# Performance work log

Measured on AMD Instinct MI355X. Metric: run time of the kernel, lower is better.

## Reference

```python
import jax, jax.numpy as jnp
import numpy as np

B, S, N, D, H, M, P_OFF = 16, 4, 2048, 128, 16, 4096, 4092


def setup_inputs() -> dict:
    key = jax.random.key(0)
    ks = jax.random.split(key, 6)
    return {
        "X": jax.random.normal(ks[0], (B, S, N), dtype=jnp.float32),
        "W_q": jax.random.normal(ks[1], (N, N), dtype=jnp.float32) * 0.02,
        "W_k": jax.random.normal(ks[2], (N, N), dtype=jnp.float32) * 0.02,
        "W_v": jax.random.normal(ks[3], (N, N), dtype=jnp.float32) * 0.02,
        "cache_K": jax.random.normal(ks[4], (B, H, M, D), dtype=jnp.float32),
        "cache_V": jax.random.normal(ks[5], (B, H, M, D), dtype=jnp.float32),
        "P": P_OFF,
    }


def reference(X, W_q, W_k, W_v, cache_K, cache_V, P):
    b, s, n = X.shape
    _, h, m, d = cache_K.shape
    # RMSNorm (no eps, no learned scale, matching the source)
    variance = jnp.mean(X * X, axis=-1, keepdims=True)
    X_norm = X * jax.lax.rsqrt(variance)
    # QKV projections -> [b, h, s, d]
    Q = (X_norm @ W_q).reshape(b, s, h, d).transpose(0, 2, 1, 3)
    K = (X_norm @ W_k).reshape(b, s, h, d).transpose(0, 2, 1, 3)
    V = (X_norm @ W_v).reshape(b, s, h, d).transpose(0, 2, 1, 3)
    # KV-cache write at static offset P
    cK = cache_K.at[:, :, P:P + s, :].set(K)
    cV = cache_V.at[:, :, P:P + s, :].set(V)
    # Attention over full cache (note: source applies no 1/sqrt(d) scale)
    scores = jnp.einsum("bhsd,bhmd->bhsm", Q, cK)
    attn = jax.nn.softmax(scores, axis=-1)
    O = jnp.einsum("bhsm,bhmd->bhsd", attn, cV)
    return O.transpose(0, 2, 1, 3).reshape(b, s, n)
```

## Files before the change

kernel.cpp:

```cpp
#include <hip/hip_runtime.h>
#include <hip/hip_bf16.h>
#include <math.h>

#define NB 16
#define NS 4
#define NN 2048
#define ND 128
#define NH 16
#define NM 4096
#define NCHK 8
#define CHROWS 512

#define XN_OFF   0u
#define Q_OFF    131072u
#define K_OFF    262144u
#define V_OFF    393216u
#define OP_OFF   524288u
#define ML_OFF   1572864u
#define PART_OFF 1589248u

__global__ __launch_bounds__(256) void k_rmsnorm(const float* __restrict__ X,
                                                 float* __restrict__ ws) {
    const int row = blockIdx.x;
    const int tid = threadIdx.x;
    const float* xr = X + (size_t)row * NN;
    float4 a = *(const float4*)(xr + tid * 4);
    float4 b = *(const float4*)(xr + 1024 + tid * 4);
    float ss = a.x*a.x + a.y*a.y + a.z*a.z + a.w*a.w
             + b.x*b.x + b.y*b.y + b.z*b.z + b.w*b.w;
    #pragma unroll
    for (int off = 32; off; off >>= 1) ss += __shfl_xor(ss, off);
    __shared__ float ls[4];
    if ((tid & 63) == 0) ls[tid >> 6] = ss;
    __syncthreads();
    const float r = rsqrtf((ls[0] + ls[1] + ls[2] + ls[3]) * (1.0f / NN));
    float* o = ws + XN_OFF + (size_t)row * NN;
    *(float4*)(o + tid * 4)        = make_float4(a.x*r, a.y*r, a.z*r, a.w*r);
    *(float4*)(o + 1024 + tid * 4) = make_float4(b.x*r, b.y*r, b.z*r, b.w*r);
}

__global__ __launch_bounds__(256) void k_qkv(const float* __restrict__ Wq,
                                             const float* __restrict__ Wk,
                                             const float* __restrict__ Wv,
                                             float* __restrict__ ws) {
    __shared__ float xsT[64][68];
    __shared__ float wt[64][132];
    const int ct    = blockIdx.x;
    const int which = blockIdx.y;
    const int kc    = blockIdx.z;
    const float* __restrict__ W = (which == 0) ? Wq : (which == 1) ? Wk : Wv;
    const int tid = threadIdx.x;
    const int c0  = ct * 128;
    const int rg  = tid >> 5;
    const int cg  = tid & 31;
    const float* xn = ws + XN_OFF;

    float4 acc[8];
    #pragma unroll
    for (int i = 0; i < 8; i++) acc[i] = make_float4(0.f, 0.f, 0.f, 0.f);

    for (int s = 0; s < 4; s++) {
        const int k0 = kc * 256 + s * 64;
        __syncthreads();
        {
            const int r  = tid >> 2;
            const int q4 = tid & 3;
            #pragma unroll
            for (int i = 0; i < 4; i++) {
                const int f4 = q4 + i * 4;
                float4 v = *(const float4*)(xn + (size_t)r * NN + k0 + f4 * 4);
                xsT[f4 * 4 + 0][r] = v.x;
                xsT[f4 * 4 + 1][r] = v.y;
                xsT[f4 * 4 + 2][r] = v.z;
                xsT[f4 * 4 + 3][r] = v.w;
            }
        }
        {
            #pragma unroll
            for (int j8 = 0; j8 < 8; j8++) {
                const int kk  = j8 * 8 + (tid >> 5);
                const int f4c = tid & 31;
                float4 v = *(const float4*)(W + (size_t)(k0 + kk) * NN + c0 + f4c * 4);
                *(float4*)&wt[kk][f4c * 4] = v;
            }
        }
        __syncthreads();
        #pragma unroll 8
        for (int kk = 0; kk < 64; kk++) {
            const float4 x0 = *(const float4*)&xsT[kk][rg * 8];
            const float4 x1 = *(const float4*)&xsT[kk][rg * 8 + 4];
            const float4 w4 = *(const float4*)&wt[kk][cg * 4];
            acc[0].x += x0.x*w4.x; acc[0].y += x0.x*w4.y; acc[0].z += x0.x*w4.z; acc[0].w += x0.x*w4.w;
            acc[1].x += x0.y*w4.x; acc[1].y += x0.y*w4.y; acc[1].z += x0.y*w4.z; acc[1].w += x0.y*w4.w;
            acc[2].x += x0.z*w4.x; acc[2].y += x0.z*w4.y; acc[2].z += x0.z*w4.z; acc[2].w += x0.z*w4.w;
            acc[3].x += x0.w*w4.x; acc[3].y += x0.w*w4.y; acc[3].z += x0.w*w4.z; acc[3].w += x0.w*w4.w;
            acc[4].x += x1.x*w4.x; acc[4].y += x1.x*w4.y; acc[4].z += x1.x*w4.z; acc[4].w += x1.x*w4.w;
            acc[5].x += x1.y*w4.x; acc[5].y += x1.y*w4.y; acc[5].z += x1.y*w4.z; acc[5].w += x1.y*w4.w;
            acc[6].x += x1.z*w4.x; acc[6].y += x1.z*w4.y; acc[6].z += x1.z*w4.z; acc[6].w += x1.z*w4.w;
            acc[7].x += x1.w*w4.x; acc[7].y += x1.w*w4.y; acc[7].z += x1.w*w4.z; acc[7].w += x1.w*w4.w;
        }
    }
    float* po = ws + PART_OFF + (size_t)(kc * 3 + which) * 131072u;
    #pragma unroll
    for (int i = 0; i < 8; i++)
        *(float4*)(po + (size_t)(rg * 8 + i) * NN + c0 + cg * 4) = acc[i];
}

__global__ __launch_bounds__(256) void k_reduce(float* __restrict__ ws) {
    const int idx = blockIdx.x * 256 + threadIdx.x;
    const int which = idx >> 15;
    const int off   = idx & 32767;
    float4 s = make_float4(0.f, 0.f, 0.f, 0.f);
    #pragma unroll
    for (int kcc = 0; kcc < 8; kcc++) {
        const float4 v = *(const float4*)(ws + PART_OFF
                         + (size_t)(kcc * 3 + which) * 131072u + (size_t)off * 4);
        s.x += v.x; s.y += v.y; s.z += v.z; s.w += v.w;
    }
    *(float4*)(ws + Q_OFF + (size_t)which * 131072u + (size_t)off * 4) = s;
}

__global__ __launch_bounds__(256) void k_attn(const float* __restrict__ cK,
                                              const float* __restrict__ cV,
                                              const int* __restrict__ Pp,
                                              float* __restrict__ ws) {
    const int ch = blockIdx.x, h = blockIdx.y, b = blockIdx.z;
    const int tid = threadIdx.x;
    const int wv = tid >> 6, lane = tid & 63;
    const int P = *Pp;
    __shared__ float Ks[2][64 * 128];
    __shared__ float Qs[4][128] __attribute__((aligned(16)));
    __shared__ float ps[64][4] __attribute__((aligned(16)));
    __shared__ float facs[4] __attribute__((aligned(16)));
    __shared__ float Ow[4][4][128];
    __shared__ float mls[4][2];

    if (tid < 128) {
        const int q = tid >> 5, d = (tid & 31) * 4;
        *(float4*)&Qs[q][d] =
            *(const float4*)(ws + Q_OFF + (size_t)(b * 4 + q) * NN + h * 128 + d);
    }

    const float* kbase = cK + (size_t)(b * NH + h) * NM * ND;
    const float* vbase = cV + (size_t)(b * NH + h) * NM * ND;
    const float* knew  = ws + K_OFF;
    const float* vnew  = ws + V_OFF;
    const int mb0 = ch * CHROWS;

    auto STAGE = [&](int tt, int bufi) {
        const int mb = mb0 + tt * 64;
        #pragma unroll
        for (int i = 0; i < 8; i++) {
            const int g0  = (wv * 8 + i) * 64;
            const int g   = g0 + lane;
            const int row = g >> 5;
            const int c4  = g & 31;
            const int csw = c4 ^ (row & 7);
            const int mrow = mb + row;
            const float* src;
            if (mrow >= P && mrow < P + NS)
                src = knew + (size_t)(b * 4 + (mrow - P)) * NN + h * 128 + csw * 4;
            else
                src = kbase + (size_t)mrow * ND + csw * 4;
            __builtin_amdgcn_global_load_lds(
                (const __attribute__((address_space(1))) void*)src,
                (__attribute__((address_space(3))) void*)(&Ks[bufi][g0 * 4]),
                16, 0, 0);
        }
    };

    float m_run = -INFINITY, l_run = 0.f;
    float2 Oa[4];
    #pragma unroll
    for (int q = 0; q < 4; q++) Oa[q] = make_float2(0.f, 0.f);

    STAGE(0, 0);
    __syncthreads();

    for (int t = 0; t < 8; t++) {
        const int cur = t & 1;
        if (t < 7) STAGE(t + 1, cur ^ 1);

        const float* kr = &Ks[cur][lane * 128];
        const int s7 = lane & 7;
        float s = 0.f;
        #pragma unroll
        for (int d4 = 0; d4 < 32; d4++) {
            const float4 k4 = *(const float4*)&kr[(d4 ^ s7) * 4];
            const float4 q4 = *(const float4*)&Qs[wv][d4 * 4];
            s += k4.x*q4.x + k4.y*q4.y + k4.z*q4.z + k4.w*q4.w;
        }
        float wm = s;
        #pragma unroll
        for (int off = 32; off; off >>= 1) wm = fmaxf(wm, __shfl_xor(wm, off));
        const float mn  = fmaxf(m_run, wm);
        const float fac = __expf(m_run - mn);
        m_run = mn;
        const float p = __expf(s - mn);
        l_run = l_run * fac + p;
        ps[lane][wv] = p;
        if (lane == 0) facs[wv] = fac;
        asm volatile("s_waitcnt lgkmcnt(0)" ::: "memory");
        __builtin_amdgcn_s_barrier();
        __builtin_amdgcn_sched_barrier(0);

        const float4 fq = *(const float4*)&facs[0];
        Oa[0].x *= fq.x; Oa[0].y *= fq.x;
        Oa[1].x *= fq.y; Oa[1].y *= fq.y;
        Oa[2].x *= fq.z; Oa[2].y *= fq.z;
        Oa[3].x *= fq.w; Oa[3].y *= fq.w;
        const int r0 = wv * 16;
        #pragma unroll 4
        for (int r = 0; r < 16; r++) {
            const int mr = mb0 + t * 64 + r0 + r;
            const float* vp = (mr >= P && mr < P + NS)
                            ? vnew + (size_t)(b * 4 + (mr - P)) * NN + h * 128
                            : vbase + (size_t)mr * ND;
            const float2 v2 = *(const float2*)(vp + lane * 2);
            const float4 pr = *(const float4*)&ps[r0 + r][0];
            Oa[0].x += pr.x * v2.x; Oa[0].y += pr.x * v2.y;
            Oa[1].x += pr.y * v2.x; Oa[1].y += pr.y * v2.y;
            Oa[2].x += pr.z * v2.x; Oa[2].y += pr.z * v2.y;
            Oa[3].x += pr.w * v2.x; Oa[3].y += pr.w * v2.y;
        }
        __syncthreads();
    }

    #pragma unroll
    for (int off = 32; off; off >>= 1) l_run += __shfl_xor(l_run, off);
    #pragma unroll
    for (int q = 0; q < 4; q++)
        *(float2*)&Ow[wv][q][lane * 2] = Oa[q];
    if (lane == 0) { mls[wv][0] = m_run; mls[wv][1] = l_run; }
    __syncthreads();

    const int q = wv;
    const int d0 = lane * 2;
    float o0 = 0.f, o1 = 0.f;
    #pragma unroll
    for (int w2 = 0; w2 < 4; w2++) {
        o0 += Ow[w2][q][d0];
        o1 += Ow[w2][q][d0 + 1];
    }
    const size_t bh = (size_t)(b * NH + h);
    const size_t pidx = ((bh * NCHK + ch) * 4 + q) * 128 + d0;
    ws[OP_OFF + pidx]     = o0;
    ws[OP_OFF + pidx + 1] = o1;
    if (lane == 0) {
        const size_t mi = ((bh * NCHK + ch) * 4 + q) * 2;
        ws[ML_OFF + mi]     = mls[q][0];
        ws[ML_OFF + mi + 1] = mls[q][1];
    }
}

__global__ __launch_bounds__(256) void k_comb(const float* __restrict__ ws,
                                              float* __restrict__ out) {
    const int bh = blockIdx.x;
    const int b = bh >> 4, h = bh & 15;
    const int tid = threadIdx.x;
    const int q = tid >> 6, d0 = (tid & 63) * 2;
    float ms = -INFINITY;
    #pragma unroll
    for (int c = 0; c < NCHK; c++)
        ms = fmaxf(ms, ws[ML_OFF + (((size_t)bh * NCHK + c) * 4 + q) * 2]);
    float o0 = 0.f, o1 = 0.f, den = 0.f;
    #pragma unroll
    for (int c = 0; c < NCHK; c++) {
        const size_t mi = (((size_t)bh * NCHK + c) * 4 + q) * 2;
        float e = __expf(ws[ML_OFF + mi] - ms);
        den += e * ws[ML_OFF + mi + 1];
        const size_t pi = (((size_t)bh * NCHK + c) * 4 + q) * 128 + d0;
        o0 += e * ws[OP_OFF + pi];
        o1 += e * ws[OP_OFF + pi + 1];
    }
    const float inv = 1.0f / den;
    const size_t oi = (size_t)(b * 4 + q) * NN + h * 128 + d0;
    *(float2*)(out + oi) = make_float2(o0 * inv, o1 * inv);
}

extern "C" void kernel_launch(void* const* d_in, const int* in_sizes, int n_in,
                              void* d_out, int out_size, void* d_ws, size_t ws_size,
                              hipStream_t stream) {
    const float* X  = (const float*)d_in[0];
    const float* Wq = (const float*)d_in[1];
    const float* Wk = (const float*)d_in[2];
    const float* Wv = (const float*)d_in[3];
    const float* cK = (const float*)d_in[4];
    const float* cV = (const float*)d_in[5];
    const int*   Pp = (const int*)d_in[6];
    float* ws = (float*)d_ws;
    float* out = (float*)d_out;

    hipLaunchKernelGGL(k_rmsnorm, dim3(64), dim3(256), 0, stream, X, ws);
    hipLaunchKernelGGL(k_qkv, dim3(16, 3, 8), dim3(256), 0, stream, Wq, Wk, Wv, ws);
    hipLaunchKernelGGL(k_reduce, dim3(384), dim3(256), 0, stream, ws);
    hipLaunchKernelGGL(k_attn, dim3(NCHK, NH, NB), dim3(256), 0, stream, cK, cV, Pp, ws);
    hipLaunchKernelGGL(k_comb, dim3(NB * NH), dim3(256), 0, stream, ws, out);
}
```

Before: 265.7 us.

## Stage V tiles through LDS asynchronously and double split-K in QKV projection

The attention kernel now prefetches V rows into double-buffered LDS alongside K with asynchronous global-to-LDS loads, replacing the synchronous per-row global V reads in the PV loop. Tiles shrink to 32 rows so both K and V buffers fit, and the QK dot product is split across half-waves then combined with a shuffle. Separately, the QKV projection uses 16 K-chunks instead of 8 to expose more blocks, at the cost of twice the partial-sum traffic in the reduce kernel. The partial buffer also doubles in size, which relies on the workspace being large enough.

```diff
diff --git a/kernel.cpp b/kernel.cpp
--- a/kernel.cpp
+++ b/kernel.cpp
@@ -10,6 +10,9 @@
 #define NM 4096
 #define NCHK 8
 #define CHROWS 512
+#define TROWS 32
+#define NT 16
+#define NKC 16
 
 #define XN_OFF   0u
 #define Q_OFF    131072u
@@ -59,8 +62,8 @@
     #pragma unroll
     for (int i = 0; i < 8; i++) acc[i] = make_float4(0.f, 0.f, 0.f, 0.f);
 
-    for (int s = 0; s < 4; s++) {
-        const int k0 = kc * 256 + s * 64;
+    for (int s = 0; s < 2; s++) {
+        const int k0 = kc * 128 + s * 64;
         __syncthreads();
         {
             const int r  = tid >> 2;
@@ -112,7 +115,7 @@
     const int off   = idx & 32767;
     float4 s = make_float4(0.f, 0.f, 0.f, 0.f);
     #pragma unroll
-    for (int kcc = 0; kcc < 8; kcc++) {
+    for (int kcc = 0; kcc < NKC; kcc++) {
         const float4 v = *(const float4*)(ws + PART_OFF
                          + (size_t)(kcc * 3 + which) * 131072u + (size_t)off * 4);
         s.x += v.x; s.y += v.y; s.z += v.z; s.w += v.w;
@@ -127,10 +130,12 @@
     const int ch = blockIdx.x, h = blockIdx.y, b = blockIdx.z;
     const int tid = threadIdx.x;
     const int wv = tid >> 6, lane = tid & 63;
+    const int half = lane >> 5, r32 = lane & 31;
     const int P = *Pp;
-    __shared__ float Ks[2][64 * 128];
+    __shared__ float Ks[2][TROWS * 128];
+    __shared__ float Vs[2][TROWS * 128];
     __shared__ float Qs[4][128] __attribute__((aligned(16)));
-    __shared__ float ps[64][4] __attribute__((aligned(16)));
+    __shared__ float ps[TROWS][4] __attribute__((aligned(16)));
     __shared__ float facs[4] __attribute__((aligned(16)));
     __shared__ float Ow[4][4][128];
     __shared__ float mls[4][2];
@@ -148,25 +153,38 @@
     const int mb0 = ch * CHROWS;
 
     auto STAGE = [&](int tt, int bufi) {
-        const int mb = mb0 + tt * 64;
-        #pragma unroll
-        for (int i = 0; i < 8; i++) {
-            const int g0  = (wv * 8 + i) * 64;
+        const int mb = mb0 + tt * TROWS;
+        #pragma unroll
+        for (int i = 0; i < 4; i++) {
+            const int g0  = (wv * 4 + i) * 64;
             const int g   = g0 + lane;
             const int row = g >> 5;
             const int c4  = g & 31;
             const int csw = c4 ^ (row & 7);
             const int mrow = mb + row;
-            const float* src;
-            if (mrow >= P && mrow < P + NS)
-                src = knew + (size_t)(b * 4 + (mrow - P)) * NN + h * 128 + csw * 4;
-            else
-                src = kbase + (size_t)mrow * ND + csw * 4;
+            const float* src = (mrow >= P && mrow < P + NS)
+                ? knew + (size_t)(b * 4 + (mrow - P)) * NN + h * 128 + csw * 4
+                : kbase + (size_t)mrow * ND + csw * 4;
             __builtin_amdgcn_global_load_lds(
                 (const __attribute__((address_space(1))) void*)src,
                 (__attribute__((address_space(3))) void*)(&Ks[bufi][g0 * 4]),
                 16, 0, 0);
         }
+        #pragma unroll
+        for (int i = 0; i < 4; i++) {
+            const int g0  = (wv * 4 + i) * 64;
+            const int g   = g0 + lane;
+            const int row = g >> 5;
+            const int c4  = g & 31;
+            const int mrow = mb + row;
+            const float* src = (mrow >= P && mrow < P + NS)
+                ? vnew + (size_t)(b * 4 + (mrow - P)) * NN + h * 128 + c4 * 4
+                : vbase + (size_t)mrow * ND + c4 * 4;
+            __builtin_amdgcn_global_load_lds(
+                (const __attribute__((address_space(1))) void*)src,
+                (__attribute__((address_space(3))) void*)(&Vs[bufi][g0 * 4]),
+                16, 0, 0);
+        }
     };
 
     float m_run = -INFINITY, l_run = 0.f;
@@ -177,28 +195,30 @@
     STAGE(0, 0);
     __syncthreads();
 
-    for (int t = 0; t < 8; t++) {
+    for (int t = 0; t < NT; t++) {
         const int cur = t & 1;
-        if (t < 7) STAGE(t + 1, cur ^ 1);
-
-        const float* kr = &Ks[cur][lane * 128];
-        const int s7 = lane & 7;
+        if (t < NT - 1) STAGE(t + 1, cur ^ 1);
+
+        const int s7 = r32 & 7;
+        const float* kr = &Ks[cur][r32 * 128 + half * 64];
+        const float* qr = &Qs[wv][half * 64];
         float s = 0.f;
         #pragma unroll
-        for (int d4 = 0; d4 < 32; d4++) {
-            const float4 k4 = *(const float4*)&kr[(d4 ^ s7) * 4];
-            const float4 q4 = *(const float4*)&Qs[wv][d4 * 4];
+        for (int j = 0; j < 16; j++) {
+            const float4 k4 = *(const float4*)&kr[(j ^ s7) * 4];
+            const float4 q4 = *(const float4*)&qr[j * 4];
             s += k4.x*q4.x + k4.y*q4.y + k4.z*q4.z + k4.w*q4.w;
         }
+        s += __shfl_xor(s, 32);
         float wm = s;
         #pragma unroll
-        for (int off = 32; off; off >>= 1) wm = fmaxf(wm, __shfl_xor(wm, off));
+        for (int off = 16; off; off >>= 1) wm = fmaxf(wm, __shfl_xor(wm, off));
         const float mn  = fmaxf(m_run, wm);
         const float fac = __expf(m_run - mn);
         m_run = mn;
         const float p = __expf(s - mn);
-        l_run = l_run * fac + p;
-        ps[lane][wv] = p;
+        l_run = l_run * fac + ((half == 0) ? p : 0.f);
+        if (half == 0) ps[r32][wv] = p;
         if (lane == 0) facs[wv] = fac;
         asm volatile("s_waitcnt lgkmcnt(0)" ::: "memory");
         __builtin_amdgcn_s_barrier();
@@ -209,15 +229,11 @@
         Oa[1].x *= fq.y; Oa[1].y *= fq.y;
         Oa[2].x *= fq.z; Oa[2].y *= fq.z;
         Oa[3].x *= fq.w; Oa[3].y *= fq.w;
-        const int r0 = wv * 16;
-        #pragma unroll 4
-        for (int r = 0; r < 16; r++) {
-            const int mr = mb0 + t * 64 + r0 + r;
-            const float* vp = (mr >= P && mr < P + NS)
-                            ? vnew + (size_t)(b * 4 + (mr - P)) * NN + h * 128
-                            : vbase + (size_t)mr * ND;
-            const float2 v2 = *(const float2*)(vp + lane * 2);
-            const float4 pr = *(const float4*)&ps[r0 + r][0];
+        const int r0 = wv * 8;
+        #pragma unroll
+        for (int rr = 0; rr < 8; rr++) {
+            const float2 v2 = *(const float2*)&Vs[cur][(r0 + rr) * 128 + lane * 2];
+            const float4 pr = *(const float4*)&ps[r0 + rr][0];
             Oa[0].x += pr.x * v2.x; Oa[0].y += pr.x * v2.y;
             Oa[1].x += pr.y * v2.x; Oa[1].y += pr.y * v2.y;
             Oa[2].x += pr.z * v2.x; Oa[2].y += pr.z * v2.y;
@@ -292,7 +308,7 @@
     float* out = (float*)d_out;
 
     hipLaunchKernelGGL(k_rmsnorm, dim3(64), dim3(256), 0, stream, X, ws);
-    hipLaunchKernelGGL(k_qkv, dim3(16, 3, 8), dim3(256), 0, stream, Wq, Wk, Wv, ws);
+    hipLaunchKernelGGL(k_qkv, dim3(16, 3, NKC), dim3(256), 0, stream, Wq, Wk, Wv, ws);
     hipLaunchKernelGGL(k_reduce, dim3(384), dim3(256), 0, stream, ws);
     hipLaunchKernelGGL(k_attn, dim3(NCHK, NH, NB), dim3(256), 0, stream, cK, cV, Pp, ws);
     hipLaunchKernelGGL(k_comb, dim3(NB * NH), dim3(256), 0, stream, ws, out);
```

New measurement: 238.2 us. 1.12x faster.
